# Optimization experiments

Hardware: AMD Instinct MI355X
Metric: run time of the kernel (lower is better)

## Reference

```python
import jax, jax.numpy as jnp
import numpy as np
from jax import lax

B, T, N, D = 16, 96, 512, 128
M, K, H = 1196, 8, 4
TAU_TIME = 2.0
KW = 12  # depthwise kernel size


def _l2norm(x, axis=-1, eps=1e-12):
    n = jnp.sqrt(jnp.sum(x * x, axis=axis, keepdims=True))
    return x / jnp.maximum(n, eps)


def setup_inputs() -> dict:
    key = jax.random.key(0)
    ks = jax.random.split(key, 20)
    hid = N * D
    inp = {
        'x_scalar': jax.random.normal(ks[0], (B, T, N), jnp.float32),
        'season_q': jax.random.randint(ks[1], (B,), 0, 4),
        'year_q': jax.random.uniform(ks[2], (B,), jnp.float32, 0.0, 10.0),
        # temporal encoder params
        'dw_w': jax.random.normal(ks[3], (N, 1, KW), jnp.float32) * 0.1,
        'dw_b': jnp.zeros((N,), jnp.float32),
        'pw_w': jax.random.normal(ks[4], (hid, N), jnp.float32) * 0.02,
        'pw_b': jnp.zeros((hid,), jnp.float32),
        'ln_g': jnp.ones((D,), jnp.float32),
        'ln_b': jnp.zeros((D,), jnp.float32),
        # multi-head attention params (torch MultiheadAttention layout)
        'in_proj_w': jax.random.normal(ks[5], (3 * D, D), jnp.float32) * 0.05,
        'in_proj_b': jnp.zeros((3 * D,), jnp.float32),
        'out_proj_w': jax.random.normal(ks[6], (D, D), jnp.float32) * 0.05,
        'out_proj_b': jnp.zeros((D,), jnp.float32),
        # final projection
        'proj_w': jax.random.normal(ks[7], (D, D), jnp.float32) * 0.05,
        'proj_b': jnp.zeros((D,), jnp.float32),
        # memory bank buffers (assume memory is full: count == M)
        'memory_bank': jax.random.normal(ks[8], (M, N, D), jnp.float32),
        'memory_seasons': jax.random.randint(ks[9], (M,), 0, 4),
        'memory_years': jax.random.uniform(ks[10], (M,), jnp.float32, 0.0, 10.0),
    }
    return inp


def _encoder(x_scalar, dw_w, dw_b, pw_w, pw_b, ln_g, ln_b):
    # x_scalar: [B,T,N] -> (with d_input=1) channels = N, layout [B,N,T]
    x = jnp.transpose(x_scalar, (0, 2, 1))
    # depthwise conv, groups=N, kernel=12, padding=6 -> length T+1
    x = lax.conv_general_dilated(x, dw_w, window_strides=(1,), padding=[(6, 6)],
                                 dimension_numbers=('NCH', 'OIH', 'NCH'),
                                 feature_group_count=N)
    x = jax.nn.gelu(x + dw_b[None, :, None], approximate=False)
    # pointwise 1x1 conv == GEMM over channels: [B, N*D, T+1]
    x = jnp.einsum('oi,bit->bot', pw_w, x) + pw_b[None, :, None]
    x = jax.nn.gelu(x, approximate=False)
    # adaptive avg pool to 1 == mean over time
    q = jnp.mean(x, axis=-1).reshape(B, N, D)
    # layernorm over last dim
    mu = jnp.mean(q, axis=-1, keepdims=True)
    var = jnp.mean((q - mu) ** 2, axis=-1, keepdims=True)
    return (q - mu) / jnp.sqrt(var + 1e-5) * ln_g + ln_b


def _retrieve(q, season_q, year_q, memory_bank, memory_seasons, memory_years):
    q_flat = _l2norm(q.reshape(B, -1))            # [B, N*D]
    mem_flat = _l2norm(memory_bank.reshape(M, -1))  # [M, N*D]
    sim = q_flat @ mem_flat.T                     # [B, M]
    season_mask = (season_q[:, None] == memory_seasons[None, :]).astype(sim.dtype)
    sim = sim * season_mask + (1.0 - season_mask) * (-10000.0)
    delta_year = jnp.abs(year_q[:, None] - memory_years[None, :])
    diversity = 1.0 - jnp.exp(-delta_year / TAU_TIME)  # gap_years == 0 path
    sim = sim * (0.5 + 0.5 * diversity)
    _, topk_idx = lax.top_k(sim, K)               # [B, K]
    return memory_bank[topk_idx]                  # [B, K, N, D]


def reference(x_scalar, season_q, year_q, dw_w, dw_b, pw_w, pw_b, ln_g, ln_b,
              in_proj_w, in_proj_b, out_proj_w, out_proj_b, proj_w, proj_b,
              memory_bank, memory_seasons, memory_years):
    q = _encoder(x_scalar, dw_w, dw_b, pw_w, pw_b, ln_g, ln_b)      # [B,N,D]
    retrieved = _retrieve(q, season_q, year_q, memory_bank, memory_seasons, memory_years)
    kv = jnp.transpose(retrieved, (0, 2, 1, 3))                      # [B,N,K,D]
    dh = D // H
    wq, wk, wv = in_proj_w[:D], in_proj_w[D:2 * D], in_proj_w[2 * D:]
    bq, bk, bv = in_proj_b[:D], in_proj_b[D:2 * D], in_proj_b[2 * D:]
    qh = (q @ wq.T + bq).reshape(B, N, H, dh)
    kh = (kv @ wk.T + bk).reshape(B, N, K, H, dh)
    vh = (kv @ wv.T + bv).reshape(B, N, K, H, dh)
    scores = jnp.einsum('bnhd,bnkhd->bnhk', qh, kh) / jnp.sqrt(jnp.asarray(dh, q.dtype))
    attn = jax.nn.softmax(scores, axis=-1)
    ctx = jnp.einsum('bnhk,bnkhd->bnhd', attn, vh).reshape(B, N, D)
    out = ctx @ out_proj_w.T + out_proj_b
    return (out @ proj_w.T + proj_b, q)
```

## Files before the change

### kernel.cpp

```cpp
#include <hip/hip_runtime.h>
#include <hip/hip_bf16.h>

#define BB_ 16
#define TT_ 96
#define NN 512
#define DD 128
#define MM 1196
#define KK 8
#define HID 65536
#define TP 97
#define TPAD 128

typedef __attribute__((ext_vector_type(8))) short short8v;
typedef __attribute__((ext_vector_type(4))) float f32x4;

__device__ __forceinline__ float gelu_exact(float x) {
    return 0.5f * x * (1.0f + erff(x * 0.70710678118654752f));
}
__device__ __forceinline__ unsigned rne16(float f) {
    unsigned u = __float_as_uint(f);
    return (u + 0x7fffu + ((u >> 16) & 1u)) >> 16;
}
__device__ __forceinline__ float bf2f(short s) {
    return __uint_as_float(((unsigned)(unsigned short)s) << 16);
}
__device__ __forceinline__ void split2(float x, short& hi, short& lo) {
    unsigned h = rne16(x);
    hi = (short)h;
    float hf = __uint_as_float(h << 16);
    lo = (short)rne16(x - hf);
}
__device__ __forceinline__ void gload_lds16(const void* g, void* l) {
    __builtin_amdgcn_global_load_lds((const __attribute__((address_space(1))) void*)g,
                                     (__attribute__((address_space(3))) void*)l, 16, 0, 0);
}
__device__ __forceinline__ short8v pack8(float4 a, float4 b) {
    short t[8];
    t[0] = (short)rne16(a.x); t[1] = (short)rne16(a.y);
    t[2] = (short)rne16(a.z); t[3] = (short)rne16(a.w);
    t[4] = (short)rne16(b.x); t[5] = (short)rne16(b.y);
    t[6] = (short)rne16(b.z); t[7] = (short)rne16(b.w);
    return *(short8v*)t;
}
__device__ __forceinline__ int swz32(int row) {
    return (row & 3) ^ ((row >> 2) & 3);
}
__device__ __forceinline__ void stage_tile_sw(const short* g, short* lds, int tid) {
    #pragma unroll
    for (int j = 0; j < 8; ++j) {
        int row = j * 16 + (tid >> 4);
        int csrc = (tid & 15) ^ (row & 7);
        gload_lds16(g + row * 128 + csrc * 8, lds + j * 2048 + tid * 8);
    }
}
__device__ __forceinline__ short8v frag_ld(const short* lds, int row, int kk, int lk) {
    return *(const short8v*)&lds[row * 128 + (((kk << 2) + lk) ^ (row & 7)) * 8];
}

__global__ __launch_bounds__(256) void k0_cvt2(const float* __restrict__ src,
                                               short* __restrict__ hi, short* __restrict__ lo) {
    size_t i = ((size_t)blockIdx.x * 256 + threadIdx.x) * 8;
    float4 a = *(const float4*)(src + i);
    float4 b = *(const float4*)(src + i + 4);
    short h[8], l[8];
    split2(a.x, h[0], l[0]); split2(a.y, h[1], l[1]);
    split2(a.z, h[2], l[2]); split2(a.w, h[3], l[3]);
    split2(b.x, h[4], l[4]); split2(b.y, h[5], l[5]);
    split2(b.z, h[6], l[6]); split2(b.w, h[7], l[7]);
    *(short8v*)(hi + i) = *(short8v*)h;
    *(short8v*)(lo + i) = *(short8v*)l;
}

__global__ __launch_bounds__(256) void k1_conv(const float* __restrict__ x,
                                               const float* __restrict__ dw_w,
                                               const float* __restrict__ dw_b,
                                               short* __restrict__ xh,
                                               short* __restrict__ xl) {
    int b = blockIdx.y, n0 = blockIdx.x * 64;
    __shared__ float xs[96][64];
    __shared__ float ws[64][12];
    __shared__ float bs[64];
    int tid = threadIdx.x;
    for (int j = tid; j < 96 * 64; j += 256) {
        int t = j / 64, n = j % 64;
        xs[t][n] = x[(size_t)(b * TT_ + t) * NN + n0 + n];
    }
    for (int j = tid; j < 64 * 12; j += 256) {
        int n = j / 12, k = j % 12;
        ws[n][k] = dw_w[(size_t)(n0 + n) * 12 + k];
    }
    if (tid < 64) bs[tid] = dw_b[n0 + tid];
    __syncthreads();
    int n = tid % 64, g = tid / 64;
    for (int t = g; t < TP; t += 4) {
        float acc = bs[n];
        #pragma unroll
        for (int k = 0; k < 12; ++k) {
            int ti = t - 6 + k;
            if (ti >= 0 && ti < 96) acc += xs[ti][n] * ws[n][k];
        }
        float v = gelu_exact(acc);
        short h, l;
        split2(v, h, l);
        size_t idx = ((size_t)b * TPAD + t) * NN + n0 + n;
        xh[idx] = h; xl[idx] = l;
    }
    for (int t = TP + g; t < TPAD; t += 4) {
        size_t idx = ((size_t)b * TPAD + t) * NN + n0 + n;
        xh[idx] = 0; xl[idx] = 0;
    }
}

template <bool PRE>
__global__ __launch_bounds__(256, 4) void k2_split(const float* __restrict__ pw_w,
                                                   const short* __restrict__ aH,
                                                   const short* __restrict__ aL,
                                                   const float* __restrict__ pw_b,
                                                   const short* __restrict__ bH,
                                                   const short* __restrict__ bL,
                                                   float* __restrict__ q_pre) {
    int wgid = blockIdx.x;
    int xcd = wgid & 7;
    int r = wgid >> 3;
    int b = r & 15;
    int o0 = (xcd * 64 + (r >> 4)) * 128;
    __shared__ short AsH[4096], AsL[4096], BsH[4096], BsL[4096];
    __shared__ float red[128][2];
    int tid = threadIdx.x;
    int l = tid & 63, w = tid >> 6;
    int wr = w >> 1, wc = w & 1;
    int lrow = l & 15, lk = l >> 4;
    const short* bHb = bH + (size_t)b * TPAD * NN;
    const short* bLb = bL + (size_t)b * TPAD * NN;

    f32x4 acc[4][4];
    #pragma unroll
    for (int m = 0; m < 4; ++m)
        #pragma unroll
        for (int n = 0; n < 4; ++n) acc[m][n] = (f32x4){0.f, 0.f, 0.f, 0.f};

    for (int it = 0; it < 16; ++it) {
        int k0 = it * 32;
        #pragma unroll
        for (int j = 0; j < 2; ++j) {
            int row = j * 64 + (tid >> 2);
            int c = tid & 3;
            int sc = c ^ swz32(row);
            int dofs = (j * 256 + tid) * 8;
            gload_lds16(bHb + (size_t)row * NN + k0 + sc * 8, &BsH[dofs]);
            gload_lds16(bLb + (size_t)row * NN + k0 + sc * 8, &BsL[dofs]);
            if constexpr (PRE) {
                gload_lds16(aH + (size_t)(o0 + row) * 512 + k0 + sc * 8, &AsH[dofs]);
                gload_lds16(aL + (size_t)(o0 + row) * 512 + k0 + sc * 8, &AsL[dofs]);
            } else {
                const float* src = pw_w + (size_t)(o0 + row) * 512 + k0 + c * 8;
                float4 v0 = *(const float4*)(src);
                float4 v1 = *(const float4*)(src + 4);
                short h[8], lo[8];
                split2(v0.x, h[0], lo[0]); split2(v0.y, h[1], lo[1]);
                split2(v0.z, h[2], lo[2]); split2(v0.w, h[3], lo[3]);
                split2(v1.x, h[4], lo[4]); split2(v1.y, h[5], lo[5]);
                split2(v1.z, h[6], lo[6]); split2(v1.w, h[7], lo[7]);
                int didx = row * 32 + (c ^ swz32(row)) * 8;
                *(short8v*)&AsH[didx] = *(short8v*)h;
                *(short8v*)&AsL[didx] = *(short8v*)lo;
            }
        }
        __syncthreads();
        short8v ah[4], al[4], bh[4], bl[4];
        #pragma unroll
        for (int m = 0; m < 4; ++m) {
            int row = wr * 64 + m * 16 + lrow;
            int idx = row * 32 + (lk ^ swz32(row)) * 8;
            ah[m] = *(const short8v*)&AsH[idx];
            al[m] = *(const short8v*)&AsL[idx];
        }
        #pragma unroll
        for (int n = 0; n < 4; ++n) {
            int row = wc * 64 + n * 16 + lrow;
            int idx = row * 32 + (lk ^ swz32(row)) * 8;
            bh[n] = *(const short8v*)&BsH[idx];
            bl[n] = *(const short8v*)&BsL[idx];
        }
        #pragma unroll
        for (int m = 0; m < 4; ++m)
            #pragma unroll
            for (int n = 0; n < 4; ++n) {
                acc[m][n] = __builtin_amdgcn_mfma_f32_16x16x32_bf16(ah[m], bh[n], acc[m][n], 0, 0, 0);
                acc[m][n] = __builtin_amdgcn_mfma_f32_16x16x32_bf16(ah[m], bl[n], acc[m][n], 0, 0, 0);
                acc[m][n] = __builtin_amdgcn_mfma_f32_16x16x32_bf16(al[m], bh[n], acc[m][n], 0, 0, 0);
            }
        __syncthreads();
    }
    #pragma unroll
    for (int m = 0; m < 4; ++m) {
        #pragma unroll
        for (int reg = 0; reg < 4; ++reg) {
            int o_loc = wr * 64 + m * 16 + lk * 4 + reg;
            float bias = pw_b[o0 + o_loc];
            float s = 0.f;
            #pragma unroll
            for (int n = 0; n < 4; ++n) {
                int t = wc * 64 + n * 16 + lrow;
                if (t < TP) s += gelu_exact(acc[m][n][reg] + bias);
            }
            s += __shfl_xor(s, 1, 64);
            s += __shfl_xor(s, 2, 64);
            s += __shfl_xor(s, 4, 64);
            s += __shfl_xor(s, 8, 64);
            if (lrow == 0) red[o_loc][wc] = s;
        }
    }
    __syncthreads();
    if (tid < 128)
        q_pre[(size_t)b * HID + o0 + tid] = (red[tid][0] + red[tid][1]) * (1.0f / 97.0f);
}

__global__ __launch_bounds__(256) void k3_ln(const float* __restrict__ q_pre,
                                             const float* __restrict__ g,
                                             const float* __restrict__ beta,
                                             float* __restrict__ qout) {
    int row = blockIdx.x * 4 + (threadIdx.x >> 6);
    int lane = threadIdx.x & 63;
    const float* src = q_pre + (size_t)row * 128;
    float v0 = src[lane], v1 = src[lane + 64];
    float s = v0 + v1;
    #pragma unroll
    for (int m = 32; m >= 1; m >>= 1) s += __shfl_xor(s, m, 64);
    float mu = s * (1.f / 128.f);
    float d0 = v0 - mu, d1 = v1 - mu;
    float vs = d0 * d0 + d1 * d1;
    #pragma unroll
    for (int m = 32; m >= 1; m >>= 1) vs += __shfl_xor(vs, m, 64);
    float rstd = rsqrtf(vs * (1.f / 128.f) + 1e-5f);
    qout[(size_t)row * 128 + lane] = d0 * rstd * g[lane] + beta[lane];
    qout[(size_t)row * 128 + lane + 64] = d1 * rstd * g[lane + 64] + beta[lane + 64];
}

__global__ __launch_bounds__(256) void k3b_qnorm(const float* __restrict__ q, float* __restrict__ qnorm) {
    int b = blockIdx.x;
    const float* src = q + (size_t)b * HID;
    float s = 0.f;
    for (int i = threadIdx.x * 4; i < HID; i += 256 * 4) {
        float4 v = *(const float4*)(src + i);
        s += v.x * v.x + v.y * v.y + v.z * v.z + v.w * v.w;
    }
    #pragma unroll
    for (int m = 32; m >= 1; m >>= 1) s += __shfl_xor(s, m, 64);
    __shared__ float red[4];
    if ((threadIdx.x & 63) == 0) red[threadIdx.x >> 6] = s;
    __syncthreads();
    if (threadIdx.x == 0) qnorm[b] = sqrtf(red[0] + red[1] + red[2] + red[3]);
}

__global__ __launch_bounds__(256) void k4_sim(const float* __restrict__ mem,
                                              const float* __restrict__ q,
                                              float* __restrict__ sim_part,
                                              float* __restrict__ nrm_part) {
    int m0 = blockIdx.x * 4;
    int isp = blockIdx.y;
    int tid = threadIdx.x;
    float acc[4][16];
    float nr[4] = {0.f, 0.f, 0.f, 0.f};
    #pragma unroll
    for (int a = 0; a < 4; ++a)
        #pragma unroll
        for (int c = 0; c < 16; ++c) acc[a][c] = 0.f;
    int ibase = isp * 16384;
    for (int it = 0; it < 16; ++it) {
        int i = ibase + (it * 256 + tid) * 4;
        float4 mv[4];
        #pragma unroll
        for (int a = 0; a < 4; ++a) {
            mv[a] = *(const float4*)(mem + (size_t)(m0 + a) * HID + i);
            nr[a] += mv[a].x * mv[a].x + mv[a].y * mv[a].y + mv[a].z * mv[a].z + mv[a].w * mv[a].w;
        }
        #pragma unroll
        for (int c = 0; c < 16; ++c) {
            float4 qv = *(const float4*)(q + (size_t)c * HID + i);
            #pragma unroll
            for (int a = 0; a < 4; ++a)
                acc[a][c] += mv[a].x * qv.x + mv[a].y * qv.y + mv[a].z * qv.z + mv[a].w * qv.w;
        }
    }
    __shared__ float red[4][68];
    int wv = tid >> 6, lane = tid & 63;
    #pragma unroll
    for (int a = 0; a < 4; ++a)
        for (int c = 0; c < 17; ++c) {
            float v = (c < 16) ? acc[a][c] : nr[a];
            #pragma unroll
            for (int m = 32; m >= 1; m >>= 1) v += __shfl_xor(v, m, 64);
            if (lane == 0) red[wv][a * 17 + c] = v;
        }
    __syncthreads();
    if (tid < 68) {
        float v = red[0][tid] + red[1][tid] + red[2][tid] + red[3][tid];
        int a = tid / 17, r = tid % 17;
        if (r < 16) sim_part[((size_t)isp * 16 + r) * MM + m0 + a] = v;
        else nrm_part[(size_t)isp * MM + m0 + a] = v;
    }
}

__global__ __launch_bounds__(256) void k5_topk(const float* __restrict__ sim_part,
                                               const float* __restrict__ nrm_part,
                                               const float* __restrict__ qnorm,
                                               const int* __restrict__ season_q,
                                               const float* __restrict__ year_q,
                                               const int* __restrict__ mem_season,
                                               const float* __restrict__ mem_year,
                                               int* __restrict__ topk) {
    int b = blockIdx.x;
    int tid = threadIdx.x;
    __shared__ float sadj[MM];
    float nq = fmaxf(qnorm[b], 1e-12f);
    int sq = season_q[b];
    float yq = year_q[b];
    for (int m = tid; m < MM; m += 256) {
        float dot = 0.f, ns = 0.f;
        #pragma unroll
        for (int p = 0; p < 4; ++p) {
            dot += sim_part[((size_t)p * 16 + b) * MM + m];
            ns += nrm_part[(size_t)p * MM + m];
        }
        float nm = fmaxf(sqrtf(ns), 1e-12f);
        float s = dot / (nq * nm);
        if (mem_season[m] != sq) s = -10000.0f;
        float dy = fabsf(yq - mem_year[m]);
        float dv = 1.0f - expf(-dy * 0.5f);
        s *= (0.5f + 0.5f * dv);
        sadj[m] = s;
    }
    __syncthreads();
    __shared__ float rv[4];
    __shared__ int ri[4];
    for (int it = 0; it < 8; ++it) {
        float bv = -INFINITY;
        int bi = -1;
        for (int m = tid; m < MM; m += 256) {
            float v = sadj[m];
            if (v > bv || (v == bv && bi >= 0 && m < bi)) { bv = v; bi = m; }
        }
        #pragma unroll
        for (int msk = 32; msk >= 1; msk >>= 1) {
            float ov = __shfl_xor(bv, msk, 64);
            int oi = __shfl_xor(bi, msk, 64);
            if (oi >= 0 && (ov > bv || (ov == bv && (bi < 0 || oi < bi)))) { bv = ov; bi = oi; }
        }
        int lane = tid & 63, wv = tid >> 6;
        if (lane == 0) { rv[wv] = bv; ri[wv] = bi; }
        __syncthreads();
        if (tid == 0) {
            float fv = rv[0]; int fi = ri[0];
            for (int w = 1; w < 4; ++w)
                if (ri[w] >= 0 && (rv[w] > fv || (rv[w] == fv && (fi < 0 || ri[w] < fi)))) { fv = rv[w]; fi = ri[w]; }
            topk[b * KK + it] = fi;
            sadj[fi] = -INFINITY;
        }
        __syncthreads();
    }
}

__global__ __launch_bounds__(256) void k6w(const float* __restrict__ in_w,
                                           const float* __restrict__ ow,
                                           const float* __restrict__ ob,
                                           const float* __restrict__ pw,
                                           const float* __restrict__ pb,
                                           short* __restrict__ WQKV16,
                                           short* __restrict__ WC16,
                                           float* __restrict__ BC) {
    __shared__ float ow_s[16384];
    int tid = threadIdx.x;
    for (int i = tid * 4; i < 16384; i += 1024)
        *(float4*)&ow_s[i] = *(const float4*)&ow[i];
    for (int i = tid * 8; i < 49152; i += 2048) {
        float4 a = *(const float4*)(in_w + i);
        float4 b = *(const float4*)(in_w + i + 4);
        *(short8v*)(WQKV16 + i) = pack8(a, b);
    }
    __syncthreads();
    int d = tid >> 1, j0 = (tid & 1) * 64;
    float accv[64];
    #pragma unroll
    for (int j = 0; j < 64; ++j) accv[j] = 0.f;
    for (int i = 0; i < 128; ++i) {
        float wv = pw[d * 128 + i];
        const float* orow = &ow_s[i * 128 + j0];
        #pragma unroll
        for (int j = 0; j < 64; ++j) accv[j] += wv * orow[j];
    }
    #pragma unroll
    for (int j = 0; j < 64; ++j) WC16[d * 128 + j0 + j] = (short)rne16(accv[j]);
    if (tid < 128) {
        float s = pb[tid];
        for (int i = 0; i < 128; ++i) s += pw[tid * 128 + i] * ob[i];
        BC[tid] = s;
    }
}

__global__ __launch_bounds__(256) void k6q(const float* __restrict__ q,
                                           const short* __restrict__ WQKV16,
                                           const float* __restrict__ in_b,
                                           short* __restrict__ QH16) {
    int b = blockIdx.y;
    int n0 = blockIdx.x * 128;
    __shared__ short As[16384], Ws[16384];
    int tid = threadIdx.x;
    int l = tid & 63, w = tid >> 6;
    int wr = w >> 1, wc = w & 1;
    int lrow = l & 15, lk = l >> 4;

    stage_tile_sw(WQKV16, Ws, tid);
    {
        int row = tid >> 1, half = tid & 1;
        const float* src = q + ((size_t)b * NN + n0 + row) * 128 + half * 64;
        #pragma unroll
        for (int cc = 0; cc < 8; ++cc) {
            float4 v0 = *(const float4*)(src + cc * 8);
            float4 v1 = *(const float4*)(src + cc * 8 + 4);
            int chunk = half * 8 + cc;
            *(short8v*)&As[row * 128 + (chunk ^ (row & 7)) * 8] = pack8(v0, v1);
        }
    }
    __syncthreads();
    f32x4 acc[4][4];
    #pragma unroll
    for (int m = 0; m < 4; ++m)
        #pragma unroll
        for (int n = 0; n < 4; ++n) acc[m][n] = (f32x4){0.f, 0.f, 0.f, 0.f};
    #pragma unroll
    for (int kk = 0; kk < 4; ++kk) {
        short8v a[4], bw[4];
        #pragma unroll
        for (int m = 0; m < 4; ++m) a[m] = frag_ld(As, wr * 64 + m * 16 + lrow, kk, lk);
        #pragma unroll
        for (int n = 0; n < 4; ++n) bw[n] = frag_ld(Ws, wc * 64 + n * 16 + lrow, kk, lk);
        #pragma unroll
        for (int m = 0; m < 4; ++m)
            #pragma unroll
            for (int n = 0; n < 4; ++n)
                acc[m][n] = __builtin_amdgcn_mfma_f32_16x16x32_bf16(a[m], bw[n], acc[m][n], 0, 0, 0);
    }
    #pragma unroll
    for (int m = 0; m < 4; ++m)
        #pragma unroll
        for (int n = 0; n < 4; ++n)
            #pragma unroll
            for (int reg = 0; reg < 4; ++reg) {
                int r = wr * 64 + m * 16 + lk * 4 + reg;
                int dco = wc * 64 + n * 16 + lrow;
                QH16[((size_t)b * NN + n0 + r) * 128 + dco] = (short)rne16(acc[m][n][reg] + in_b[dco]);
            }
}

__global__ __launch_bounds__(256) void k6kv(const float* __restrict__ mem,
                                            const int* __restrict__ topk,
                                            const short* __restrict__ WQKV16,
                                            const float* __restrict__ in_b,
                                            short* __restrict__ KH16,
                                            short* __restrict__ VH16) {
    int b = blockIdx.y;
    int n0 = blockIdx.x * 16;
    __shared__ short As[16384], WkS[16384], WvS[16384];
    __shared__ int idx_s[8];
    int tid = threadIdx.x;
    int l = tid & 63, w = tid >> 6;
    int wr = w >> 1, wc = w & 1;
    int lrow = l & 15, lk = l >> 4;
    if (tid < 8) idx_s[tid] = topk[b * 8 + tid];
    stage_tile_sw(WQKV16 + 16384, WkS, tid);
    stage_tile_sw(WQKV16 + 32768, WvS, tid);
    __syncthreads();
    {
        int row = tid >> 1, half = tid & 1;
        int n = n0 + (row >> 3), k = row & 7;
        const float* src = mem + (size_t)idx_s[k] * HID + (size_t)n * 128 + half * 64;
        #pragma unroll
        for (int cc = 0; cc < 8; ++cc) {
            float4 v0 = *(const float4*)(src + cc * 8);
            float4 v1 = *(const float4*)(src + cc * 8 + 4);
            int chunk = half * 8 + cc;
            *(short8v*)&As[row * 128 + (chunk ^ (row & 7)) * 8] = pack8(v0, v1);
        }
    }
    __syncthreads();
    f32x4 ak_[4][4], av_[4][4];
    #pragma unroll
    for (int m = 0; m < 4; ++m)
        #pragma unroll
        for (int n = 0; n < 4; ++n) {
            ak_[m][n] = (f32x4){0.f, 0.f, 0.f, 0.f};
            av_[m][n] = (f32x4){0.f, 0.f, 0.f, 0.f};
        }
    #pragma unroll
    for (int kk = 0; kk < 4; ++kk) {
        short8v a[4], bk[4], bv[4];
        #pragma unroll
        for (int m = 0; m < 4; ++m) a[m] = frag_ld(As, wr * 64 + m * 16 + lrow, kk, lk);
        #pragma unroll
        for (int n = 0; n < 4; ++n) {
            bk[n] = frag_ld(WkS, wc * 64 + n * 16 + lrow, kk, lk);
            bv[n] = frag_ld(WvS, wc * 64 + n * 16 + lrow, kk, lk);
        }
        #pragma unroll
        for (int m = 0; m < 4; ++m)
            #pragma unroll
            for (int n = 0; n < 4; ++n) {
                ak_[m][n] = __builtin_amdgcn_mfma_f32_16x16x32_bf16(a[m], bk[n], ak_[m][n], 0, 0, 0);
                av_[m][n] = __builtin_amdgcn_mfma_f32_16x16x32_bf16(a[m], bv[n], av_[m][n], 0, 0, 0);
            }
    }
    #pragma unroll
    for (int m = 0; m < 4; ++m)
        #pragma unroll
        for (int n = 0; n < 4; ++n)
            #pragma unroll
            for (int reg = 0; reg < 4; ++reg) {
                int r = wr * 64 + m * 16 + lk * 4 + reg;
                int dco = wc * 64 + n * 16 + lrow;
                int nl = r >> 3, k = r & 7;
                size_t o = (((size_t)b * NN + n0 + nl) * 8 + k) * 128 + dco;
                KH16[o] = (short)rne16(ak_[m][n][reg] + in_b[128 + dco]);
                VH16[o] = (short)rne16(av_[m][n][reg] + in_b[256 + dco]);
            }
}

__global__ __launch_bounds__(256) void k6s(const short* __restrict__ QH16,
                                           const short* __restrict__ KH16,
                                           const short* __restrict__ VH16,
                                           short* __restrict__ CTX16) {
    int b = blockIdx.y;
    int n = blockIdx.x * 8 + (threadIdx.x >> 5);
    int dh = threadIdx.x & 31;
    size_t qbase = ((size_t)b * NN + n) * 128;
    size_t kvbase = qbase * 8;
    #pragma unroll
    for (int h = 0; h < 4; ++h) {
        int d = h * 32 + dh;
        float qv = bf2f(QH16[qbase + d]);
        float sc[8];
        #pragma unroll
        for (int k = 0; k < 8; ++k) {
            float p = qv * bf2f(KH16[kvbase + k * 128 + d]);
            #pragma unroll
            for (int m = 16; m >= 1; m >>= 1) p += __shfl_xor(p, m, 32);
            sc[k] = p * 0.17677669529663687f;
        }
        float mx = sc[0];
        #pragma unroll
        for (int k = 1; k < 8; ++k) mx = fmaxf(mx, sc[k]);
        float den = 0.f;
        #pragma unroll
        for (int k = 0; k < 8; ++k) { sc[k] = expf(sc[k] - mx); den += sc[k]; }
        float inv = 1.0f / den;
        float c = 0.f;
        #pragma unroll
        for (int k = 0; k < 8; ++k) c += sc[k] * bf2f(VH16[kvbase + k * 128 + d]);
        CTX16[qbase + d] = (short)rne16(c * inv);
    }
}

__global__ __launch_bounds__(256) void k6f(const short* __restrict__ CTX16,
                                           const short* __restrict__ WC16,
                                           const float* __restrict__ BC,
                                           float* __restrict__ out) {
    int r0 = blockIdx.x * 128;
    __shared__ short As[16384], Ws[16384];
    int tid = threadIdx.x;
    int l = tid & 63, w = tid >> 6;
    int wr = w >> 1, wc = w & 1;
    int lrow = l & 15, lk = l >> 4;
    stage_tile_sw(CTX16 + (size_t)r0 * 128, As, tid);
    stage_tile_sw(WC16, Ws, tid);
    __syncthreads();
    f32x4 acc[4][4];
    #pragma unroll
    for (int m = 0; m < 4; ++m)
        #pragma unroll
        for (int n = 0; n < 4; ++n) acc[m][n] = (f32x4){0.f, 0.f, 0.f, 0.f};
    #pragma unroll
    for (int kk = 0; kk < 4; ++kk) {
        short8v a[4], bw[4];
        #pragma unroll
        for (int m = 0; m < 4; ++m) a[m] = frag_ld(As, wr * 64 + m * 16 + lrow, kk, lk);
        #pragma unroll
        for (int n = 0; n < 4; ++n) bw[n] = frag_ld(Ws, wc * 64 + n * 16 + lrow, kk, lk);
        #pragma unroll
        for (int m = 0; m < 4; ++m)
            #pragma unroll
            for (int n = 0; n < 4; ++n)
                acc[m][n] = __builtin_amdgcn_mfma_f32_16x16x32_bf16(a[m], bw[n], acc[m][n], 0, 0, 0);
    }
    #pragma unroll
    for (int m = 0; m < 4; ++m)
        #pragma unroll
        for (int n = 0; n < 4; ++n)
            #pragma unroll
            for (int reg = 0; reg < 4; ++reg) {
                int r = wr * 64 + m * 16 + lk * 4 + reg;
                int dco = wc * 64 + n * 16 + lrow;
                out[(size_t)(r0 + r) * 128 + dco] = acc[m][n][reg] + BC[dco];
            }
}

__global__ __launch_bounds__(256) void k6_attn(const float* __restrict__ mem,
                                               const float* __restrict__ q,
                                               const int* __restrict__ topk,
                                               const float* __restrict__ in_w,
                                               const float* __restrict__ in_b,
                                               const float* __restrict__ ow,
                                               const float* __restrict__ ob,
                                               const float* __restrict__ pw,
                                               const float* __restrict__ pb,
                                               float* __restrict__ out) {
    int b = blockIdx.y;
    int n0 = blockIdx.x * 4;
    int tid = threadIdx.x;
    __shared__ float kv_s[4][8][128];
    __shared__ float kh_s[4][8][128];
    __shared__ float vh_s[4][8][128];
    __shared__ float qin_s[4][128];
    __shared__ float qh_s[4][128];
    __shared__ float ctx_s[4][128];
    __shared__ float o1_s[4][128];
    __shared__ int idx_s[8];
    if (tid < 8) idx_s[tid] = topk[b * 8 + tid];
    __syncthreads();
    for (int j = tid; j < 4 * 8 * 32; j += 256) {
        int n = j >> 8;
        int k = (j >> 5) & 7;
        int d4 = (j & 31) * 4;
        float4 v = *(const float4*)(mem + (size_t)idx_s[k] * HID + (size_t)(n0 + n) * 128 + d4);
        *(float4*)&kv_s[n][k][d4] = v;
    }
    for (int j = tid; j < 4 * 32; j += 256) {
        int n = j >> 5;
        int d4 = (j & 31) * 4;
        *(float4*)&qin_s[n][d4] = *(const float4*)(q + (size_t)(b * NN + n0 + n) * 128 + d4);
    }
    __syncthreads();
    {
        int d = tid & 127, half = tid >> 7;
        for (int n2 = 0; n2 < 2; ++n2) {
            int n = half * 2 + n2;
            float a = in_b[d];
            const float* wr = in_w + (size_t)d * 128;
            #pragma unroll
            for (int i = 0; i < 128; i += 4) {
                float4 w4 = *(const float4*)(wr + i);
                a += w4.x * qin_s[n][i] + w4.y * qin_s[n][i + 1] + w4.z * qin_s[n][i + 2] + w4.w * qin_s[n][i + 3];
            }
            qh_s[n][d] = a;
        }
    }
    {
        int d = tid & 127, layer = tid >> 7;
        float ak[16], av[16];
        #pragma unroll
        for (int p = 0; p < 16; ++p) { ak[p] = in_b[128 + d]; av[p] = in_b[256 + d]; }
        const float* wkr = in_w + (size_t)(128 + d) * 128;
        const float* wvr = in_w + (size_t)(256 + d) * 128;
        for (int i = 0; i < 128; i += 4) {
            float4 wk4 = *(const float4*)(wkr + i);
            float4 wv4 = *(const float4*)(wvr + i);
            #pragma unroll
            for (int p = 0; p < 16; ++p) {
                int pg = layer * 16 + p;
                int n = pg >> 3, k = pg & 7;
                float4 x4 = *(const float4*)&kv_s[n][k][i];
                ak[p] += wk4.x * x4.x + wk4.y * x4.y + wk4.z * x4.z + wk4.w * x4.w;
                av[p] += wv4.x * x4.x + wv4.y * x4.y + wv4.z * x4.z + wv4.w * x4.w;
            }
        }
        #pragma unroll
        for (int p = 0; p < 16; ++p) {
            int pg = layer * 16 + p;
            int n = pg >> 3, k = pg & 7;
            kh_s[n][k][d] = ak[p];
            vh_s[n][k][d] = av[p];
        }
    }
    __syncthreads();
    {
        int n = tid >> 6, lane = tid & 63;
        int dh = lane & 31, hh = lane >> 5;
        #pragma unroll
        for (int hp = 0; hp < 2; ++hp) {
            int h = hp * 2 + hh;
            int dd0 = h * 32 + dh;
            float qv = qh_s[n][dd0];
            float sc[8];
            #pragma unroll
            for (int k = 0; k < 8; ++k) {
                float p = qv * kh_s[n][k][dd0];
                #pragma unroll
                for (int msk = 16; msk >= 1; msk >>= 1) p += __shfl_xor(p, msk, 32);
                sc[k] = p * 0.17677669529663687f;
            }
            float mx = sc[0];
            #pragma unroll
            for (int k = 1; k < 8; ++k) mx = fmaxf(mx, sc[k]);
            float den = 0.f;
            #pragma unroll
            for (int k = 0; k < 8; ++k) { sc[k] = expf(sc[k] - mx); den += sc[k]; }
            float inv = 1.0f / den;
            float c = 0.f;
            #pragma unroll
            for (int k = 0; k < 8; ++k) c += sc[k] * vh_s[n][k][dd0];
            ctx_s[n][dd0] = c * inv;
        }
    }
    __syncthreads();
    {
        int d = tid & 127, half = tid >> 7;
        for (int n2 = 0; n2 < 2; ++n2) {
            int n = half * 2 + n2;
            float a = ob[d];
            const float* wr = ow + (size_t)d * 128;
            #pragma unroll
            for (int i = 0; i < 128; i += 4) {
                float4 w4 = *(const float4*)(wr + i);
                a += w4.x * ctx_s[n][i] + w4.y * ctx_s[n][i + 1] + w4.z * ctx_s[n][i + 2] + w4.w * ctx_s[n][i + 3];
            }
            o1_s[n][d] = a;
        }
    }
    __syncthreads();
    {
        int d = tid & 127, half = tid >> 7;
        for (int n2 = 0; n2 < 2; ++n2) {
            int n = half * 2 + n2;
            float a = pb[d];
            const float* wr = pw + (size_t)d * 128;
            #pragma unroll
            for (int i = 0; i < 128; i += 4) {
                float4 w4 = *(const float4*)(wr + i);
                a += w4.x * o1_s[n][i] + w4.y * o1_s[n][i + 1] + w4.z * o1_s[n][i + 2] + w4.w * o1_s[n][i + 3];
            }
            out[(size_t)(b * NN + n0 + n) * 128 + d] = a;
        }
    }
}

extern "C" void kernel_launch(void* const* d_in, const int* in_sizes, int n_in,
                              void* d_out, int out_size, void* d_ws, size_t ws_size,
                              hipStream_t stream) {
    const float* x_scalar   = (const float*)d_in[0];
    const int*   season_q   = (const int*)d_in[1];
    const float* year_q     = (const float*)d_in[2];
    const float* dw_w       = (const float*)d_in[3];
    const float* dw_b       = (const float*)d_in[4];
    const float* pw_w       = (const float*)d_in[5];
    const float* pw_b       = (const float*)d_in[6];
    const float* ln_g       = (const float*)d_in[7];
    const float* ln_bb      = (const float*)d_in[8];
    const float* in_proj_w  = (const float*)d_in[9];
    const float* in_proj_b  = (const float*)d_in[10];
    const float* out_proj_w = (const float*)d_in[11];
    const float* out_proj_b = (const float*)d_in[12];
    const float* proj_w     = (const float*)d_in[13];
    const float* proj_b     = (const float*)d_in[14];
    const float* memory_bank= (const float*)d_in[15];
    const int*   mem_season = (const int*)d_in[16];
    const float* mem_year   = (const float*)d_in[17];

    float* out_final = (float*)d_out;
    float* q_out = out_final + (size_t)BB_ * NN * DD;

    float* ws = (float*)d_ws;
    size_t off = 0;
    float* QPRE  = ws + off; off += 1048576;
    float* QNORM = ws + off; off += 16;
    float* NRMP  = ws + off; off += 4 * MM;
    float* SIMP  = ws + off; off += 64 * MM;
    int*   TOPK  = (int*)(ws + off); off += 128;
    short* XH    = (short*)(ws + off); off += 524288;
    short* XL    = (short*)(ws + off); off += 524288;
    short* AH    = (short*)(ws + off); off += 16777216;
    short* AL    = (short*)(ws + off); off += 16777216;
    bool use_pre = (ws_size >= off * 4);

    short* WQKV16 = AH;
    short* WC16   = AH + 49152;
    float* BC     = (float*)(AH + 65536);
    short* QH16   = AH + 66048;
    short* KH16   = QH16 + 1048576;
    short* VH16   = KH16 + 8388608;
    short* CTX16  = VH16 + 8388608;

    k1_conv<<<dim3(8, 16), 256, 0, stream>>>(x_scalar, dw_w, dw_b, XH, XL);
    if (use_pre) {
        k0_cvt2<<<16384, 256, 0, stream>>>(pw_w, AH, AL);
        k2_split<true><<<8192, 256, 0, stream>>>(pw_w, AH, AL, pw_b, XH, XL, QPRE);
    } else {
        k2_split<false><<<8192, 256, 0, stream>>>(pw_w, nullptr, nullptr, pw_b, XH, XL, QPRE);
    }
    k3_ln<<<2048, 256, 0, stream>>>(QPRE, ln_g, ln_bb, q_out);
    k3b_qnorm<<<16, 256, 0, stream>>>(q_out, QNORM);
    k4_sim<<<dim3(299, 4), 256, 0, stream>>>(memory_bank, q_out, SIMP, NRMP);
    k5_topk<<<16, 256, 0, stream>>>(SIMP, NRMP, QNORM, season_q, year_q, mem_season, mem_year, TOPK);
    if (use_pre) {
        k6w<<<1, 256, 0, stream>>>(in_proj_w, out_proj_w, out_proj_b, proj_w, proj_b, WQKV16, WC16, BC);
        k6q<<<dim3(4, 16), 256, 0, stream>>>(q_out, WQKV16, in_proj_b, QH16);
        k6kv<<<dim3(32, 16), 256, 0, stream>>>(memory_bank, TOPK, WQKV16, in_proj_b, KH16, VH16);
        k6s<<<dim3(64, 16), 256, 0, stream>>>(QH16, KH16, VH16, CTX16);
        k6f<<<64, 256, 0, stream>>>(CTX16, WC16, BC, out_final);
    } else {
        k6_attn<<<dim3(128, 16), 256, 0, stream>>>(memory_bank, q_out, TOPK, in_proj_w, in_proj_b,
                                                   out_proj_w, out_proj_b, proj_w, proj_b, out_final);
    }
}
```

Before: 703.3 us.

## Fuse pw_w bf16 hi/lo split into pointwise GEMM and merge hi/lo LDS tiles

Drops the separate pass that converted the 64K×512 pointwise weight into bf16 hi/lo arrays in workspace. The GEMM kernel now loads fp32 weights directly and splits them in registers using packed v_cvt_pk_bf16_f32. It stores hi and lo halves side by side in a single swizzled 64-short-wide LDS row, and B tiles are laid out the same way. This removes a full extra write and read of about 128MB of converted weights plus a kernel launch. In exchange, the conversion arithmetic runs inside each GEMM block, and each weight row is re-converted by the 16 batch blocks that share it.

```diff
diff --git a/kernel.cpp b/kernel.cpp
--- a/kernel.cpp
+++ b/kernel.cpp
@@ -30,6 +30,16 @@
     float hf = __uint_as_float(h << 16);
     lo = (short)rne16(x - hf);
 }
+__device__ __forceinline__ void splitpk(float a, float b, unsigned& h, unsigned& lo) {
+    unsigned r;
+    asm("v_cvt_pk_bf16_f32 %0, %1, %2" : "=v"(r) : "v"(a), "v"(b));
+    float ha = __uint_as_float(r << 16);
+    float hb = __uint_as_float(r & 0xffff0000u);
+    float la = a - ha, lb = b - hb;
+    unsigned r2;
+    asm("v_cvt_pk_bf16_f32 %0, %1, %2" : "=v"(r2) : "v"(la), "v"(lb));
+    h = r; lo = r2;
+}
 __device__ __forceinline__ void gload_lds16(const void* g, void* l) {
     __builtin_amdgcn_global_load_lds((const __attribute__((address_space(1))) void*)g,
                                      (__attribute__((address_space(3))) void*)l, 16, 0, 0);
@@ -42,9 +52,6 @@
     t[6] = (short)rne16(b.z); t[7] = (short)rne16(b.w);
     return *(short8v*)t;
 }
-__device__ __forceinline__ int swz32(int row) {
-    return (row & 3) ^ ((row >> 2) & 3);
-}
 __device__ __forceinline__ void stage_tile_sw(const short* g, short* lds, int tid) {
     #pragma unroll
     for (int j = 0; j < 8; ++j) {
@@ -56,19 +63,8 @@
 __device__ __forceinline__ short8v frag_ld(const short* lds, int row, int kk, int lk) {
     return *(const short8v*)&lds[row * 128 + (((kk << 2) + lk) ^ (row & 7)) * 8];
 }
-
-__global__ __launch_bounds__(256) void k0_cvt2(const float* __restrict__ src,
-                                               short* __restrict__ hi, short* __restrict__ lo) {
-    size_t i = ((size_t)blockIdx.x * 256 + threadIdx.x) * 8;
-    float4 a = *(const float4*)(src + i);
-    float4 b = *(const float4*)(src + i + 4);
-    short h[8], l[8];
-    split2(a.x, h[0], l[0]); split2(a.y, h[1], l[1]);
-    split2(a.z, h[2], l[2]); split2(a.w, h[3], l[3]);
-    split2(b.x, h[4], l[4]); split2(b.y, h[5], l[5]);
-    split2(b.z, h[6], l[6]); split2(b.w, h[7], l[7]);
-    *(short8v*)(hi + i) = *(short8v*)h;
-    *(short8v*)(lo + i) = *(short8v*)l;
+__device__ __forceinline__ short8v frag32(const short* lds, int row, int c) {
+    return *(const short8v*)&lds[row * 64 + ((c ^ (row & 7)) * 8)];
 }
 
 __global__ __launch_bounds__(256) void k1_conv(const float* __restrict__ x,
@@ -111,20 +107,17 @@
     }
 }
 
-template <bool PRE>
-__global__ __launch_bounds__(256, 4) void k2_split(const float* __restrict__ pw_w,
-                                                   const short* __restrict__ aH,
-                                                   const short* __restrict__ aL,
-                                                   const float* __restrict__ pw_b,
-                                                   const short* __restrict__ bH,
-                                                   const short* __restrict__ bL,
-                                                   float* __restrict__ q_pre) {
+__global__ __launch_bounds__(256, 4) void k2f(const float* __restrict__ pw_w,
+                                              const float* __restrict__ pw_b,
+                                              const short* __restrict__ bH,
+                                              const short* __restrict__ bL,
+                                              float* __restrict__ q_pre) {
     int wgid = blockIdx.x;
     int xcd = wgid & 7;
     int r = wgid >> 3;
     int b = r & 15;
     int o0 = (xcd * 64 + (r >> 4)) * 128;
-    __shared__ short AsH[4096], AsL[4096], BsH[4096], BsL[4096];
+    __shared__ short As[8192], Bs[8192];
     __shared__ float red[128][2];
     int tid = threadIdx.x;
     int l = tid & 63, w = tid >> 6;
@@ -142,45 +135,42 @@
     for (int it = 0; it < 16; ++it) {
         int k0 = it * 32;
         #pragma unroll
+        for (int j = 0; j < 4; ++j) {
+            int row = j * 32 + (tid >> 3);
+            int c = (tid & 7) ^ (row & 7);
+            const short* src = (c < 4) ? bHb + (size_t)row * NN + k0 + c * 8
+                                       : bLb + (size_t)row * NN + k0 + (c - 4) * 8;
+            gload_lds16(src, &Bs[j * 2048 + tid * 8]);
+        }
+        #pragma unroll
         for (int j = 0; j < 2; ++j) {
-            int row = j * 64 + (tid >> 2);
-            int c = tid & 3;
-            int sc = c ^ swz32(row);
-            int dofs = (j * 256 + tid) * 8;
-            gload_lds16(bHb + (size_t)row * NN + k0 + sc * 8, &BsH[dofs]);
-            gload_lds16(bLb + (size_t)row * NN + k0 + sc * 8, &BsL[dofs]);
-            if constexpr (PRE) {
-                gload_lds16(aH + (size_t)(o0 + row) * 512 + k0 + sc * 8, &AsH[dofs]);
-                gload_lds16(aL + (size_t)(o0 + row) * 512 + k0 + sc * 8, &AsL[dofs]);
-            } else {
-                const float* src = pw_w + (size_t)(o0 + row) * 512 + k0 + c * 8;
-                float4 v0 = *(const float4*)(src);
-                float4 v1 = *(const float4*)(src + 4);
-                short h[8], lo[8];
-                split2(v0.x, h[0], lo[0]); split2(v0.y, h[1], lo[1]);
-                split2(v0.z, h[2], lo[2]); split2(v0.w, h[3], lo[3]);
-                split2(v1.x, h[4], lo[4]); split2(v1.y, h[5], lo[5]);
-                split2(v1.z, h[6], lo[6]); split2(v1.w, h[7], lo[7]);
-                int didx = row * 32 + (c ^ swz32(row)) * 8;
-                *(short8v*)&AsH[didx] = *(short8v*)h;
-                *(short8v*)&AsL[didx] = *(short8v*)lo;
-            }
+            int row = j * 64 + l;
+            const float* srcA = pw_w + (size_t)(o0 + row) * 512 + k0 + w * 8;
+            float4 v0 = *(const float4*)(srcA);
+            float4 v1 = *(const float4*)(srcA + 4);
+            unsigned h01, l01, h23, l23, h45, l45, h67, l67;
+            splitpk(v0.x, v0.y, h01, l01);
+            splitpk(v0.z, v0.w, h23, l23);
+            splitpk(v1.x, v1.y, h45, l45);
+            splitpk(v1.z, v1.w, h67, l67);
+            uint4 hv = make_uint4(h01, h23, h45, h67);
+            uint4 lv = make_uint4(l01, l23, l45, l67);
+            *(uint4*)&As[row * 64 + ((w ^ (row & 7)) * 8)] = hv;
+            *(uint4*)&As[row * 64 + (((w + 4) ^ (row & 7)) * 8)] = lv;
         }
         __syncthreads();
         short8v ah[4], al[4], bh[4], bl[4];
         #pragma unroll
         for (int m = 0; m < 4; ++m) {
             int row = wr * 64 + m * 16 + lrow;
-            int idx = row * 32 + (lk ^ swz32(row)) * 8;
-            ah[m] = *(const short8v*)&AsH[idx];
-            al[m] = *(const short8v*)&AsL[idx];
+            ah[m] = frag32(As, row, lk);
+            al[m] = frag32(As, row, lk + 4);
         }
         #pragma unroll
         for (int n = 0; n < 4; ++n) {
             int row = wc * 64 + n * 16 + lrow;
-            int idx = row * 32 + (lk ^ swz32(row)) * 8;
-            bh[n] = *(const short8v*)&BsH[idx];
-            bl[n] = *(const short8v*)&BsL[idx];
+            bh[n] = frag32(Bs, row, lk);
+            bl[n] = frag32(Bs, row, lk + 4);
         }
         #pragma unroll
         for (int m = 0; m < 4; ++m)
@@ -776,30 +766,25 @@
     int*   TOPK  = (int*)(ws + off); off += 128;
     short* XH    = (short*)(ws + off); off += 524288;
     short* XL    = (short*)(ws + off); off += 524288;
-    short* AH    = (short*)(ws + off); off += 16777216;
-    short* AL    = (short*)(ws + off); off += 16777216;
-    bool use_pre = (ws_size >= off * 4);
-
-    short* WQKV16 = AH;
-    short* WC16   = AH + 49152;
-    float* BC     = (float*)(AH + 65536);
-    short* QH16   = AH + 66048;
+
+    short* ATT    = (short*)(ws + off);
+    short* WQKV16 = ATT;
+    short* WC16   = ATT + 49152;
+    float* BC     = (float*)(ATT + 65536);
+    short* QH16   = ATT + 66048;
     short* KH16   = QH16 + 1048576;
     short* VH16   = KH16 + 8388608;
     short* CTX16  = VH16 + 8388608;
+    size_t attn_shorts = 66048 + 1048576 + 8388608 + 8388608 + 1048576;
+    bool split_attn = (ws_size >= off * 4 + attn_shorts * 2);
 
     k1_conv<<<dim3(8, 16), 256, 0, stream>>>(x_scalar, dw_w, dw_b, XH, XL);
-    if (use_pre) {
-        k0_cvt2<<<16384, 256, 0, stream>>>(pw_w, AH, AL);
-        k2_split<true><<<8192, 256, 0, stream>>>(pw_w, AH, AL, pw_b, XH, XL, QPRE);
-    } else {
-        k2_split<false><<<8192, 256, 0, stream>>>(pw_w, nullptr, nullptr, pw_b, XH, XL, QPRE);
-    }
+    k2f<<<8192, 256, 0, stream>>>(pw_w, pw_b, XH, XL, QPRE);
     k3_ln<<<2048, 256, 0, stream>>>(QPRE, ln_g, ln_bb, q_out);
     k3b_qnorm<<<16, 256, 0, stream>>>(q_out, QNORM);
     k4_sim<<<dim3(299, 4), 256, 0, stream>>>(memory_bank, q_out, SIMP, NRMP);
     k5_topk<<<16, 256, 0, stream>>>(SIMP, NRMP, QNORM, season_q, year_q, mem_season, mem_year, TOPK);
-    if (use_pre) {
+    if (split_attn) {
         k6w<<<1, 256, 0, stream>>>(in_proj_w, out_proj_w, out_proj_b, proj_w, proj_b, WQKV16, WC16, BC);
         k6q<<<dim3(4, 16), 256, 0, stream>>>(q_out, WQKV16, in_proj_b, QH16);
         k6kv<<<dim3(32, 16), 256, 0, stream>>>(memory_bank, TOPK, WQKV16, in_proj_b, KH16, VH16);
```

Measured after the change: 713.0 us. Within noise of the previous version (+1.4%).

## Fuse qnorm into LayerNorm, fuse attention softmax into final GEMM, skip padded rows

Applied to the files above, without the earlier changes.

The per-batch query norm is now accumulated with atomics inside the LayerNorm kernel, so the separate qnorm kernel is gone. Its accumulator is zeroed inside the conv kernel. The attention softmax/context kernel is merged into the final projection GEMM, so context rows are written straight into swizzled LDS and never round-trip through global memory. The pointwise GEMM also skips loading and running MFMAs on padded time rows past 112. The cost is that the fused attention kernel launches only 64 blocks, which lowers parallelism for the softmax phase, and the atomics make the norm sum order nondeterministic.

```diff
diff --git a/kernel.cpp b/kernel.cpp
--- a/kernel.cpp
+++ b/kernel.cpp
@@ -75,12 +75,14 @@
                                                const float* __restrict__ dw_w,
                                                const float* __restrict__ dw_b,
                                                short* __restrict__ xh,
-                                               short* __restrict__ xl) {
+                                               short* __restrict__ xl,
+                                               float* __restrict__ qnorm2) {
     int b = blockIdx.y, n0 = blockIdx.x * 64;
     __shared__ float xs[96][64];
     __shared__ float ws[64][12];
     __shared__ float bs[64];
     int tid = threadIdx.x;
+    if (blockIdx.x == 0 && blockIdx.y == 0 && tid < 16) qnorm2[tid] = 0.f;
     for (int j = tid; j < 96 * 64; j += 256) {
         int t = j / 64, n = j % 64;
         xs[t][n] = x[(size_t)(b * TT_ + t) * NN + n0 + n];
@@ -147,8 +149,10 @@
             int c = tid & 3;
             int sc = c ^ swz32(row);
             int dofs = (j * 256 + tid) * 8;
-            gload_lds16(bHb + (size_t)row * NN + k0 + sc * 8, &BsH[dofs]);
-            gload_lds16(bLb + (size_t)row * NN + k0 + sc * 8, &BsL[dofs]);
+            if (!(j == 1 && (tid >> 2) >= 48)) {
+                gload_lds16(bHb + (size_t)row * NN + k0 + sc * 8, &BsH[dofs]);
+                gload_lds16(bLb + (size_t)row * NN + k0 + sc * 8, &BsL[dofs]);
+            }
             if constexpr (PRE) {
                 gload_lds16(aH + (size_t)(o0 + row) * 512 + k0 + sc * 8, &AsH[dofs]);
                 gload_lds16(aL + (size_t)(o0 + row) * 512 + k0 + sc * 8, &AsL[dofs]);
@@ -177,6 +181,7 @@
         }
         #pragma unroll
         for (int n = 0; n < 4; ++n) {
+            if (wc == 1 && n == 3) continue;
             int row = wc * 64 + n * 16 + lrow;
             int idx = row * 32 + (lk ^ swz32(row)) * 8;
             bh[n] = *(const short8v*)&BsH[idx];
@@ -186,6 +191,7 @@
         for (int m = 0; m < 4; ++m)
             #pragma unroll
             for (int n = 0; n < 4; ++n) {
+                if (wc == 1 && n == 3) continue;
                 acc[m][n] = __builtin_amdgcn_mfma_f32_16x16x32_bf16(ah[m], bh[n], acc[m][n], 0, 0, 0);
                 acc[m][n] = __builtin_amdgcn_mfma_f32_16x16x32_bf16(ah[m], bl[n], acc[m][n], 0, 0, 0);
                 acc[m][n] = __builtin_amdgcn_mfma_f32_16x16x32_bf16(al[m], bh[n], acc[m][n], 0, 0, 0);
@@ -219,7 +225,8 @@
 __global__ __launch_bounds__(256) void k3_ln(const float* __restrict__ q_pre,
                                              const float* __restrict__ g,
                                              const float* __restrict__ beta,
-                                             float* __restrict__ qout) {
+                                             float* __restrict__ qout,
+                                             float* __restrict__ qnorm2) {
     int row = blockIdx.x * 4 + (threadIdx.x >> 6);
     int lane = threadIdx.x & 63;
     const float* src = q_pre + (size_t)row * 128;
@@ -233,24 +240,14 @@
     #pragma unroll
     for (int m = 32; m >= 1; m >>= 1) vs += __shfl_xor(vs, m, 64);
     float rstd = rsqrtf(vs * (1.f / 128.f) + 1e-5f);
-    qout[(size_t)row * 128 + lane] = d0 * rstd * g[lane] + beta[lane];
-    qout[(size_t)row * 128 + lane + 64] = d1 * rstd * g[lane + 64] + beta[lane + 64];
-}
-
-__global__ __launch_bounds__(256) void k3b_qnorm(const float* __restrict__ q, float* __restrict__ qnorm) {
-    int b = blockIdx.x;
-    const float* src = q + (size_t)b * HID;
-    float s = 0.f;
-    for (int i = threadIdx.x * 4; i < HID; i += 256 * 4) {
-        float4 v = *(const float4*)(src + i);
-        s += v.x * v.x + v.y * v.y + v.z * v.z + v.w * v.w;
-    }
-    #pragma unroll
-    for (int m = 32; m >= 1; m >>= 1) s += __shfl_xor(s, m, 64);
-    __shared__ float red[4];
-    if ((threadIdx.x & 63) == 0) red[threadIdx.x >> 6] = s;
-    __syncthreads();
-    if (threadIdx.x == 0) qnorm[b] = sqrtf(red[0] + red[1] + red[2] + red[3]);
+    float o0 = d0 * rstd * g[lane] + beta[lane];
+    float o1 = d1 * rstd * g[lane + 64] + beta[lane + 64];
+    qout[(size_t)row * 128 + lane] = o0;
+    qout[(size_t)row * 128 + lane + 64] = o1;
+    float ss = o0 * o0 + o1 * o1;
+    #pragma unroll
+    for (int m = 32; m >= 1; m >>= 1) ss += __shfl_xor(ss, m, 64);
+    if (lane == 0) atomicAdd(&qnorm2[row >> 9], ss);
 }
 
 __global__ __launch_bounds__(256) void k4_sim(const float* __restrict__ mem,
@@ -304,7 +301,7 @@
 
 __global__ __launch_bounds__(256) void k5_topk(const float* __restrict__ sim_part,
                                                const float* __restrict__ nrm_part,
-                                               const float* __restrict__ qnorm,
+                                               const float* __restrict__ qnorm2,
                                                const int* __restrict__ season_q,
                                                const float* __restrict__ year_q,
                                                const int* __restrict__ mem_season,
@@ -313,7 +310,7 @@
     int b = blockIdx.x;
     int tid = threadIdx.x;
     __shared__ float sadj[MM];
-    float nq = fmaxf(qnorm[b], 1e-12f);
+    float nq = fmaxf(sqrtf(qnorm2[b]), 1e-12f);
     int sq = season_q[b];
     float yq = year_q[b];
     for (int m = tid; m < MM; m += 256) {
@@ -525,53 +522,54 @@
             }
 }
 
-__global__ __launch_bounds__(256) void k6s(const short* __restrict__ QH16,
-                                           const short* __restrict__ KH16,
-                                           const short* __restrict__ VH16,
-                                           short* __restrict__ CTX16) {
-    int b = blockIdx.y;
-    int n = blockIdx.x * 8 + (threadIdx.x >> 5);
-    int dh = threadIdx.x & 31;
-    size_t qbase = ((size_t)b * NN + n) * 128;
-    size_t kvbase = qbase * 8;
-    #pragma unroll
-    for (int h = 0; h < 4; ++h) {
-        int d = h * 32 + dh;
-        float qv = bf2f(QH16[qbase + d]);
-        float sc[8];
-        #pragma unroll
-        for (int k = 0; k < 8; ++k) {
-            float p = qv * bf2f(KH16[kvbase + k * 128 + d]);
-            #pragma unroll
-            for (int m = 16; m >= 1; m >>= 1) p += __shfl_xor(p, m, 32);
-            sc[k] = p * 0.17677669529663687f;
-        }
-        float mx = sc[0];
-        #pragma unroll
-        for (int k = 1; k < 8; ++k) mx = fmaxf(mx, sc[k]);
-        float den = 0.f;
-        #pragma unroll
-        for (int k = 0; k < 8; ++k) { sc[k] = expf(sc[k] - mx); den += sc[k]; }
-        float inv = 1.0f / den;
-        float c = 0.f;
-        #pragma unroll
-        for (int k = 0; k < 8; ++k) c += sc[k] * bf2f(VH16[kvbase + k * 128 + d]);
-        CTX16[qbase + d] = (short)rne16(c * inv);
-    }
-}
-
-__global__ __launch_bounds__(256) void k6f(const short* __restrict__ CTX16,
-                                           const short* __restrict__ WC16,
-                                           const float* __restrict__ BC,
-                                           float* __restrict__ out) {
+__global__ __launch_bounds__(256) void k6sf(const short* __restrict__ QH16,
+                                            const short* __restrict__ KH16,
+                                            const short* __restrict__ VH16,
+                                            const short* __restrict__ WC16,
+                                            const float* __restrict__ BC,
+                                            float* __restrict__ out) {
     int r0 = blockIdx.x * 128;
     __shared__ short As[16384], Ws[16384];
     int tid = threadIdx.x;
     int l = tid & 63, w = tid >> 6;
     int wr = w >> 1, wc = w & 1;
     int lrow = l & 15, lk = l >> 4;
-    stage_tile_sw(CTX16 + (size_t)r0 * 128, As, tid);
     stage_tile_sw(WC16, Ws, tid);
+    {
+        int lrow8 = tid >> 5;
+        int dh = tid & 31;
+        for (int pass = 0; pass < 16; ++pass) {
+            int row = pass * 8 + lrow8;
+            size_t gr = (size_t)(r0 + row);
+            size_t qbase = gr * 128;
+            size_t kvbase = gr * 1024;
+            #pragma unroll
+            for (int h = 0; h < 4; ++h) {
+                int d = h * 32 + dh;
+                float qv = bf2f(QH16[qbase + d]);
+                float sc[8];
+                #pragma unroll
+                for (int k = 0; k < 8; ++k) {
+                    float p = qv * bf2f(KH16[kvbase + k * 128 + d]);
+                    #pragma unroll
+                    for (int m = 16; m >= 1; m >>= 1) p += __shfl_xor(p, m, 32);
+                    sc[k] = p * 0.17677669529663687f;
+                }
+                float mx = sc[0];
+                #pragma unroll
+                for (int k = 1; k < 8; ++k) mx = fmaxf(mx, sc[k]);
+                float den = 0.f;
+                #pragma unroll
+                for (int k = 0; k < 8; ++k) { sc[k] = expf(sc[k] - mx); den += sc[k]; }
+                float inv = 1.0f / den;
+                float c = 0.f;
+                #pragma unroll
+                for (int k = 0; k < 8; ++k) c += sc[k] * bf2f(VH16[kvbase + k * 128 + d]);
+                int chunk = d >> 3;
+                As[row * 128 + ((chunk ^ (row & 7)) * 8) + (d & 7)] = (short)rne16(c * inv);
+            }
+        }
+    }
     __syncthreads();
     f32x4 acc[4][4];
     #pragma unroll
@@ -770,7 +768,7 @@
     float* ws = (float*)d_ws;
     size_t off = 0;
     float* QPRE  = ws + off; off += 1048576;
-    float* QNORM = ws + off; off += 16;
+    float* QNORM2= ws + off; off += 16;
     float* NRMP  = ws + off; off += 4 * MM;
     float* SIMP  = ws + off; off += 64 * MM;
     int*   TOPK  = (int*)(ws + off); off += 128;
@@ -786,25 +784,22 @@
     short* QH16   = AH + 66048;
     short* KH16   = QH16 + 1048576;
     short* VH16   = KH16 + 8388608;
-    short* CTX16  = VH16 + 8388608;
-
-    k1_conv<<<dim3(8, 16), 256, 0, stream>>>(x_scalar, dw_w, dw_b, XH, XL);
+
+    k1_conv<<<dim3(8, 16), 256, 0, stream>>>(x_scalar, dw_w, dw_b, XH, XL, QNORM2);
     if (use_pre) {
         k0_cvt2<<<16384, 256, 0, stream>>>(pw_w, AH, AL);
         k2_split<true><<<8192, 256, 0, stream>>>(pw_w, AH, AL, pw_b, XH, XL, QPRE);
     } else {
         k2_split<false><<<8192, 256, 0, stream>>>(pw_w, nullptr, nullptr, pw_b, XH, XL, QPRE);
     }
-    k3_ln<<<2048, 256, 0, stream>>>(QPRE, ln_g, ln_bb, q_out);
-    k3b_qnorm<<<16, 256, 0, stream>>>(q_out, QNORM);
+    k3_ln<<<2048, 256, 0, stream>>>(QPRE, ln_g, ln_bb, q_out, QNORM2);
     k4_sim<<<dim3(299, 4), 256, 0, stream>>>(memory_bank, q_out, SIMP, NRMP);
-    k5_topk<<<16, 256, 0, stream>>>(SIMP, NRMP, QNORM, season_q, year_q, mem_season, mem_year, TOPK);
+    k5_topk<<<16, 256, 0, stream>>>(SIMP, NRMP, QNORM2, season_q, year_q, mem_season, mem_year, TOPK);
     if (use_pre) {
         k6w<<<1, 256, 0, stream>>>(in_proj_w, out_proj_w, out_proj_b, proj_w, proj_b, WQKV16, WC16, BC);
         k6q<<<dim3(4, 16), 256, 0, stream>>>(q_out, WQKV16, in_proj_b, QH16);
         k6kv<<<dim3(32, 16), 256, 0, stream>>>(memory_bank, TOPK, WQKV16, in_proj_b, KH16, VH16);
-        k6s<<<dim3(64, 16), 256, 0, stream>>>(QH16, KH16, VH16, CTX16);
-        k6f<<<64, 256, 0, stream>>>(CTX16, WC16, BC, out_final);
+        k6sf<<<64, 256, 0, stream>>>(QH16, KH16, VH16, WC16, BC, out_final);
     } else {
         k6_attn<<<dim3(128, 16), 256, 0, stream>>>(memory_bank, q_out, TOPK, in_proj_w, in_proj_b,
                                                    out_proj_w, out_proj_b, proj_w, proj_b, out_final);
```

Measured after the change: 1.856 ms. +163.9%, slower.
